# Performance work log

Hardware: AMD Instinct MI355X
Metric: run time of the kernel (lower is better)

The kernel has to match this reference:

```python
import jax, jax.numpy as jnp
import numpy as np

HEIGHT, WIDTH = 224, 224
SIGMA = 3e-4      # soft-coverage falloff (DIB-R style delta)
EPS = 1e-10


def setup_inputs() -> dict:
    key = jax.random.key(0)
    kp, kf, kc = jax.random.split(key, 3)
    B, P, F = 2, 2048, 256
    points = 0.5 * jax.random.normal(kp, (B, P, 3), dtype=jnp.float32)
    faces = jax.random.randint(kf, (F, 3), 0, P, dtype=jnp.int32)
    colors = jax.random.uniform(kc, (B, P, 3), dtype=jnp.float32)
    rot = jnp.broadcast_to(jnp.eye(3, dtype=jnp.float32), (B, 3, 3))
    pos = jnp.tile(jnp.array([0.0, 0.0, 2.5], jnp.float32), (B, 1))
    tanfov = float(np.tan(45.0 * np.pi / 360.0))
    proj = jnp.array([[1.0 / tanfov], [1.0 / tanfov], [-1.0]], jnp.float32)
    return dict(points_bxpx3=points, faces_fx3=faces, camera_rot=rot,
                camera_pos=pos, camera_proj=proj, colors_bxpx3=colors)


def _render(points_bxpx3, camera_rot, camera_pos, camera_proj, colors_bxpx3, faces_fx3):
    H, W = HEIGHT, WIDTH
    # ---- perspective projection (kaolin DIB-R convention) ----
    pc = jnp.einsum('bpj,bij->bpi', points_bxpx3 - camera_pos[:, None, :], camera_rot)  # camera space [B,P,3]
    xyz = pc * camera_proj.reshape(1, 1, 3)
    xy = xyz[..., :2] / xyz[..., 2:3]                                   # NDC xy [B,P,2]
    i0, i1, i2 = faces_fx3[:, 0], faces_fx3[:, 1], faces_fx3[:, 2]
    p0, p1, p2 = pc[:, i0], pc[:, i1], pc[:, i2]                        # [B,F,3]
    q0, q1, q2 = xy[:, i0], xy[:, i1], xy[:, i2]                        # [B,F,2]
    normal = jnp.cross(p1 - p0, p2 - p0)                                # [B,F,3]
    normalz = normal[..., 2]
    normal1 = normal / jnp.sqrt(jnp.sum(normal * normal, -1, keepdims=True) + EPS)
    # ---- per-face vertex features: 3 verts x (rgb + mask) == color_bxfx12 ----
    ones = jnp.ones(colors_bxpx3.shape[:2] + (1,), colors_bxpx3.dtype)
    cm = jnp.concatenate([colors_bxpx3, ones], -1)                      # [B,P,4]
    feat = jnp.stack([cm[:, i0], cm[:, i1], cm[:, i2]], axis=2)         # [B,F,3,4]
    # ---- rasterize: per-pixel per-face barycentric test ----
    xs = (2.0 * jnp.arange(W, dtype=jnp.float32) + 1.0) / W - 1.0
    ys = 1.0 - (2.0 * jnp.arange(H, dtype=jnp.float32) + 1.0) / H
    PX = xs[None, None, :, None]                                        # [1,1,W,1]
    PY = ys[None, :, None, None]                                        # [1,H,1,1]
    bf = lambda a: a[:, None, None, :]                                  # [B,F] -> [B,1,1,F]
    x0, y0 = q0[..., 0], q0[..., 1]
    x1, y1 = q1[..., 0], q1[..., 1]
    x2, y2 = q2[..., 0], q2[..., 1]
    denom = (y1 - y2) * (x0 - x2) + (x2 - x1) * (y0 - y2)
    denom = jnp.where(jnp.abs(denom) < EPS, EPS, denom)
    dx2 = PX - bf(x2)
    dy2 = PY - bf(y2)
    lam0 = (bf(y1 - y2) * dx2 + bf(x2 - x1) * dy2) / bf(denom)          # [B,H,W,F]
    lam1 = (bf(y2 - y0) * dx2 + bf(x0 - x2) * dy2) / bf(denom)
    lam2 = 1.0 - lam0 - lam1
    inside = (lam0 >= 0) & (lam1 >= 0) & (lam2 >= 0)
    front = (normalz > 0)[:, None, None, :]
    valid = inside & front
    # nearest face: camera looks down -z, nearer == larger camera-space z
    zpix = lam0 * bf(p0[..., 2]) + lam1 * bf(p1[..., 2]) + lam2 * bf(p2[..., 2])
    score = jnp.where(valid, zpix, -1e10)
    idx = jnp.argmax(score, axis=-1)                                    # [B,H,W]
    valid_any = jnp.any(valid, axis=-1)
    take = lambda a: jnp.take_along_axis(a, idx[..., None], axis=-1)[..., 0]
    l0, l1, l2 = take(lam0), take(lam1), take(lam2)
    fsel = jax.vmap(lambda f, i: f[i])(feat, idx)                       # [B,H,W,3,4]
    imfeat = (l0[..., None] * fsel[..., 0, :] + l1[..., None] * fsel[..., 1, :]
              + l2[..., None] * fsel[..., 2, :]) * valid_any[..., None]
    # ---- soft coverage probability: dist to nearest edge, 0 inside ----
    def seg_d2(ax, ay, bx, by):
        ex, ey = bf(bx - ax), bf(by - ay)
        pax, pay = PX - bf(ax), PY - bf(ay)
        t = jnp.clip((pax * ex + pay * ey) / (ex * ex + ey * ey + EPS), 0.0, 1.0)
        ddx, ddy = pax - t * ex, pay - t * ey
        return ddx * ddx + ddy * ddy
    d2 = jnp.minimum(seg_d2(x0, y0, x1, y1),
                     jnp.minimum(seg_d2(x1, y1, x2, y2), seg_d2(x2, y2, x0, y0)))
    d2 = jnp.where(inside, 0.0, d2)
    prob = jnp.where(front, jnp.exp(-d2 / SIGMA) * (1.0 - 1e-7), 0.0)
    improb = (1.0 - jnp.exp(jnp.sum(jnp.log1p(-prob), axis=-1)))[..., None]  # [B,H,W,1]
    imrender = imfeat[..., :3]
    return imrender, improb, normal1


def reference(points_bxpx3, camera_rot, camera_pos, camera_proj, colors_bxpx3, faces_fx3):
    return _render(points_bxpx3, camera_rot, camera_pos, camera_proj, colors_bxpx3, faces_fx3)
```

## Files before the change

### kernel.cpp

```cpp
#include <hip/hip_runtime.h>
#include <math.h>

#define HGT 224
#define WID 224
#define NPIX (HGT * WID)
#define SIGMA 0.0003f
#define EPSV 1e-10f
#define FILT_STRIDE 16
#define DATA_STRIDE 32
#define MARGIN 0.062f
#define HALFDIAG 0.04420f
#define BAND (MARGIN + HALFDIAG)
#define HD_IN (HALFDIAG + 1.0e-4f)


__global__ void face_pre(const float* __restrict__ points,
                         const int* __restrict__ faces,
                         const float* __restrict__ rot,
                         const float* __restrict__ pos,
                         const float* __restrict__ proj,
                         const float* __restrict__ colors,
                         float* __restrict__ filt,
                         float* __restrict__ data,
                         float* __restrict__ out_normal,
                         int B, int P, int F) {
    int gid = blockIdx.x * blockDim.x + threadIdx.x;
    if (gid >= B * F) return;
    int b = gid / F;
    int f = gid - b * F;

    const float* Rb = rot + b * 9;
    float posx = pos[b * 3 + 0], posy = pos[b * 3 + 1], posz = pos[b * 3 + 2];
    float pj0 = proj[0], pj1 = proj[1], pj2 = proj[2];

    float pcx[3], pcy[3], pcz[3], qx[3], qy[3], col[9];
    for (int v = 0; v < 3; v++) {
        int i = faces[f * 3 + v];
        float dx = points[(b * P + i) * 3 + 0] - posx;
        float dy = points[(b * P + i) * 3 + 1] - posy;
        float dz = points[(b * P + i) * 3 + 2] - posz;
        pcx[v] = Rb[0] * dx + Rb[1] * dy + Rb[2] * dz;
        pcy[v] = Rb[3] * dx + Rb[4] * dy + Rb[5] * dz;
        pcz[v] = Rb[6] * dx + Rb[7] * dy + Rb[8] * dz;
        float zz = pcz[v] * pj2;
        qx[v] = (pcx[v] * pj0) / zz;
        qy[v] = (pcy[v] * pj1) / zz;
        col[v * 3 + 0] = colors[(b * P + i) * 3 + 0];
        col[v * 3 + 1] = colors[(b * P + i) * 3 + 1];
        col[v * 3 + 2] = colors[(b * P + i) * 3 + 2];
    }

    float ux = pcx[1] - pcx[0], uy = pcy[1] - pcy[0], uz = pcz[1] - pcz[0];
    float vx = pcx[2] - pcx[0], vy = pcy[2] - pcy[0], vz = pcz[2] - pcz[0];
    float nx = uy * vz - uz * vy;
    float ny = uz * vx - ux * vz;
    float nz = ux * vy - uy * vx;
    float ninv = 1.0f / sqrtf(nx * nx + ny * ny + nz * nz + EPSV);
    out_normal[gid * 3 + 0] = nx * ninv;
    out_normal[gid * 3 + 1] = ny * ninv;
    out_normal[gid * 3 + 2] = nz * ninv;

    float x0 = qx[0], y0 = qy[0], x1 = qx[1], y1 = qy[1], x2 = qx[2], y2 = qy[2];
    float denom = (y1 - y2) * (x0 - x2) + (x2 - x1) * (y0 - y2);
    if (fabsf(denom) < EPSV) denom = EPSV;
    float rd = 1.0f / denom;

    float a00 = (y1 - y2) * rd;
    float a01 = (x2 - x1) * rd;
    float a10 = (y2 - y0) * rd;
    float a11 = (x0 - x2) * rd;

    float z0 = pcz[0], z1 = pcz[1], z2c = pcz[2];
    float zgx = a00 * (z0 - z2c) + a10 * (z1 - z2c);
    float zgy = a01 * (z0 - z2c) + a11 * (z1 - z2c);
    float zc  = z2c - zgx * x2 - zgy * y2;

    float* fq = filt + gid * FILT_STRIDE;
    bool front = nz > 0.0f;
    fq[0] = front ? fminf(x0, fminf(x1, x2)) :  1e30f;
    fq[1] = front ? fminf(y0, fminf(y1, y2)) :  1e30f;
    fq[2] = front ? fmaxf(x0, fmaxf(x1, x2)) : -1e30f;
    fq[3] = front ? fmaxf(y0, fmaxf(y1, y2)) : -1e30f;

    float n0 = 1.0f / sqrtf(a00 * a00 + a01 * a01 + EPSV);
    float n1 = 1.0f / sqrtf(a10 * a10 + a11 * a11 + EPSV);
    float g2x = -(a00 + a10), g2y = -(a01 + a11);
    float n2 = 1.0f / sqrtf(g2x * g2x + g2y * g2y + EPSV);
    fq[4] = a00 * n0;
    fq[5] = a01 * n0;
    fq[6] = -(a00 * x2 + a01 * y2) * n0;
    fq[7] = a10 * n1;
    fq[8] = a11 * n1;
    fq[9] = -(a10 * x2 + a11 * y2) * n1;
    fq[10] = g2x * n2;
    fq[11] = g2y * n2;
    fq[12] = (1.0f - g2x * x2 - g2y * y2) * n2;
    fq[13] = zgx; fq[14] = zgy; fq[15] = zc;

    float* fp = data + gid * DATA_STRIDE;
    fp[0] = x2; fp[1] = y2;
    fp[2] = zgx; fp[3] = zgy; fp[4] = z2c;
    fp[5] = a00; fp[6] = a01; fp[7] = a10; fp[8] = a11;
    fp[9] = x0; fp[10] = y0; fp[11] = x1; fp[12] = y1;

    float e01x = x1 - x0, e01y = y1 - y0;
    float e12x = x2 - x1, e12y = y2 - y1;
    float e20x = x0 - x2, e20y = y0 - y2;
    fp[13] = e01x; fp[14] = e01y; fp[15] = 1.0f / (e01x * e01x + e01y * e01y + EPSV);
    fp[16] = e12x; fp[17] = e12y; fp[18] = 1.0f / (e12x * e12x + e12y * e12y + EPSV);
    fp[19] = e20x; fp[20] = e20y; fp[21] = 1.0f / (e20x * e20x + e20y * e20y + EPSV);
    for (int k = 0; k < 9; k++) fp[22 + k] = col[k];
    fp[31] = 0.0f;
}

__device__ __forceinline__ float seg_d2(float px, float py, float ax, float ay,
                                        float ex, float ey, float inv) {
    float pax = px - ax, pay = py - ay;
    float t = (pax * ex + pay * ey) * inv;
    t = fminf(fmaxf(t, 0.0f), 1.0f);
    float ddx = pax - t * ex;
    float ddy = pay - t * ey;
    return ddx * ddx + ddy * ddy;
}

__global__ __launch_bounds__(256) void rast(const float* __restrict__ filt,
                                            const float* __restrict__ data,
                                            float* __restrict__ out,
                                            int B, int F) {
    const int tiles_x = WID / 8;
    const int tiles_per_batch = tiles_x * (HGT / 8);
    int b = blockIdx.x / tiles_per_batch;
    int tile = blockIdx.x - b * tiles_per_batch;
    int ty = tile / tiles_x;
    int tx = tile - ty * tiles_x;

    int t = threadIdx.x & 63;
    int w = threadIdx.x >> 6;
    int lx = t & 7, ly = t >> 3;
    int x = tx * 8 + lx;
    int y = ty * 8 + ly;
    float px = (2.0f * (float)x + 1.0f) / (float)WID - 1.0f;
    float py = 1.0f - (2.0f * (float)y + 1.0f) / (float)HGT;

    float txlo = (2.0f * (float)(tx * 8) + 1.0f) / (float)WID - 1.0f - MARGIN;
    float txhi = (2.0f * (float)(tx * 8 + 7) + 1.0f) / (float)WID - 1.0f + MARGIN;
    float tyhi = 1.0f - (2.0f * (float)(ty * 8) + 1.0f) / (float)HGT + MARGIN;
    float tylo = 1.0f - (2.0f * (float)(ty * 8 + 7) + 1.0f) / (float)HGT - MARGIN;
    float cx = (16.0f * (float)tx + 8.0f) / (float)WID - 1.0f;
    float cy = 1.0f - (16.0f * (float)ty + 8.0f) / (float)HGT;

    const float* fltb = filt + (size_t)b * F * FILT_STRIDE;
    const float* datb = data + (size_t)b * F * DATA_STRIDE;

    int chunk = (F + 3) >> 2;
    int fbeg = w * chunk;
    int fend = min(fbeg + chunk, F);

    float best = -1e10f;
    int bidx = -1;
    float prod = 1.0f;
    int n_in = 0;

    for (int base = fbeg; base < fend; base += 64) {
        bool pass = false, inclass = false;
        float zgx = 0.0f, zgy = 0.0f, zc = 0.0f;
        int fl = base + t;
        if (fl < fend) {
            const float* fq = fltb + fl * FILT_STRIDE;
            float4 bb = *(const float4*)fq;
            float4 e0 = *(const float4*)(fq + 4);
            float4 e1 = *(const float4*)(fq + 8);
            float4 e2 = *(const float4*)(fq + 12);
            bool bpass = (bb.x <= txhi) & (bb.z >= txlo) & (bb.y <= tyhi) & (bb.w >= tylo);
            float d0 = e0.x * cx + e0.y * cy + e0.z;
            float d1 = e0.w * cx + e1.x * cy + e1.y;
            float d2 = e1.z * cx + e1.w * cy + e2.x;
            float dmin = fminf(d0, fminf(d1, d2));
            pass = bpass & (dmin >= -BAND);
            inclass = bpass & (dmin >= HD_IN);
            zgx = e2.y; zgy = e2.z; zc = e2.w;
        }
        unsigned long long mask_in = __ballot(inclass);
        unsigned long long mask_bd = __ballot(pass) & ~mask_in;

        n_in += (int)__popcll(mask_in);
        while (mask_in) {
            int fo = (int)__builtin_ctzll(mask_in);
            mask_in &= mask_in - 1;
            float zx = __shfl(zgx, fo);
            float zy = __shfl(zgy, fo);
            float zk = __shfl(zc,  fo);
            float zpix = zx * px + zy * py + zk;
            if (zpix > best) { best = zpix; bidx = base + fo; }
        }

        while (mask_bd) {
            int fo = (int)__builtin_ctzll(mask_bd);
            mask_bd &= mask_bd - 1;
            int fi = base + fo;
            const float* fp = datb + fi * DATA_STRIDE;

            float dx2 = px - fp[0], dy2 = py - fp[1];
            float lam0 = fp[5] * dx2 + fp[6] * dy2;
            float lam1 = fp[7] * dx2 + fp[8] * dy2;
            float lam2 = 1.0f - lam0 - lam1;
            bool inside = (lam0 >= 0.0f) && (lam1 >= 0.0f) && (lam2 >= 0.0f);

            float zpix = fp[2] * dx2 + fp[3] * dy2 + fp[4];
            if (inside && zpix > best) { best = zpix; bidx = fi; }

            float dA = seg_d2(px, py, fp[9],  fp[10], fp[13], fp[14], fp[15]);
            float dB = seg_d2(px, py, fp[11], fp[12], fp[16], fp[17], fp[18]);
            float dC = seg_d2(px, py, fp[0],  fp[1],  fp[19], fp[20], fp[21]);
            float d2 = inside ? 0.0f : fminf(dA, fminf(dB, dC));
            float pr = __expf(d2 * (-1.0f / SIGMA)) * (1.0f - 1e-7f);
            prod *= (1.0f - pr);
        }
    }

    prod *= exp2f(-24.0f * (float)n_in);

    __shared__ float sc[256], sp[256];
    __shared__ int sidx[256];
    sc[threadIdx.x] = best;
    sp[threadIdx.x] = prod;
    sidx[threadIdx.x] = bidx;
    __syncthreads();

    if (w == 0) {
        best = -1e10f; bidx = -1;
        prod = 1.0f;
        for (int k = 0; k < 4; k++) {
            int j = k * 64 + t;
            prod *= sp[j];
            float v = sc[j];
            if (v > best) {
                best = v; bidx = sidx[j];
            }
        }

        float r = 0.0f, g = 0.0f, bb = 0.0f;
        if (bidx >= 0) {
            const float* fp = datb + bidx * DATA_STRIDE;
            float dx2 = px - fp[0], dy2 = py - fp[1];
            float lam0 = fp[5] * dx2 + fp[6] * dy2;
            float lam1 = fp[7] * dx2 + fp[8] * dy2;
            float lam2 = 1.0f - lam0 - lam1;
            r  = lam0 * fp[22] + lam1 * fp[25] + lam2 * fp[28];
            g  = lam0 * fp[23] + lam1 * fp[26] + lam2 * fp[29];
            bb = lam0 * fp[24] + lam1 * fp[27] + lam2 * fp[30];
        }

        int pixidx = b * NPIX + y * WID + x;
        out[pixidx * 3 + 0] = r;
        out[pixidx * 3 + 1] = g;
        out[pixidx * 3 + 2] = bb;
        out[B * NPIX * 3 + pixidx] = 1.0f - prod;
    }
}

extern "C" void kernel_launch(void* const* d_in, const int* in_sizes, int n_in,
                              void* d_out, int out_size, void* d_ws, size_t ws_size,
                              hipStream_t stream) {
    const float* points = (const float*)d_in[0];
    const int*   faces  = (const int*)d_in[1];
    const float* rot    = (const float*)d_in[2];
    const float* pos    = (const float*)d_in[3];
    const float* proj   = (const float*)d_in[4];
    const float* colors = (const float*)d_in[5];
    float* out = (float*)d_out;

    int F = in_sizes[1] / 3;
    int B = in_sizes[3] / 3;
    int P = in_sizes[0] / (3 * B);

    float* filt = (float*)d_ws;
    float* data = filt + (size_t)B * F * FILT_STRIDE;
    float* out_normal = out + B * NPIX * 3 + B * NPIX;

    int nf = B * F;
    face_pre<<<(nf + 255) / 256, 256, 0, stream>>>(points, faces, rot, pos, proj,
                                                   colors, filt, data, out_normal,
                                                   B, P, F);

    int blocks = B * (NPIX / 64);
    rast<<<blocks, 256, 0, stream>>>(filt, data, out, B, F);
}
```

Baseline: 77.70 us.

## Stage per-face data in LDS and store filter records structure-of-arrays

```diff
diff --git a/kernel.cpp b/kernel.cpp
--- a/kernel.cpp
+++ b/kernel.cpp
@@ -6,8 +6,9 @@
 #define NPIX (HGT * WID)
 #define SIGMA 0.0003f
 #define EPSV 1e-10f
-#define FILT_STRIDE 16
 #define DATA_STRIDE 32
+#define LDS_STRIDE 33
+#define MAXF 256
 #define MARGIN 0.062f
 #define HALFDIAG 0.04420f
 #define BAND (MARGIN + HALFDIAG)
@@ -75,27 +76,28 @@
     float zgy = a01 * (z0 - z2c) + a11 * (z1 - z2c);
     float zc  = z2c - zgx * x2 - zgy * y2;
 
-    float* fq = filt + gid * FILT_STRIDE;
+    int BF = B * F;
+    float4* f4 = (float4*)filt;
     bool front = nz > 0.0f;
-    fq[0] = front ? fminf(x0, fminf(x1, x2)) :  1e30f;
-    fq[1] = front ? fminf(y0, fminf(y1, y2)) :  1e30f;
-    fq[2] = front ? fmaxf(x0, fmaxf(x1, x2)) : -1e30f;
-    fq[3] = front ? fmaxf(y0, fmaxf(y1, y2)) : -1e30f;
+    if (front) {
+        f4[0 * BF + gid] = make_float4(fminf(x0, fminf(x1, x2)),
+                                       fminf(y0, fminf(y1, y2)),
+                                       fmaxf(x0, fmaxf(x1, x2)),
+                                       fmaxf(y0, fmaxf(y1, y2)));
+    } else {
+        f4[0 * BF + gid] = make_float4(1e30f, 1e30f, -1e30f, -1e30f);
+    }
 
     float n0 = 1.0f / sqrtf(a00 * a00 + a01 * a01 + EPSV);
     float n1 = 1.0f / sqrtf(a10 * a10 + a11 * a11 + EPSV);
     float g2x = -(a00 + a10), g2y = -(a01 + a11);
     float n2 = 1.0f / sqrtf(g2x * g2x + g2y * g2y + EPSV);
-    fq[4] = a00 * n0;
-    fq[5] = a01 * n0;
-    fq[6] = -(a00 * x2 + a01 * y2) * n0;
-    fq[7] = a10 * n1;
-    fq[8] = a11 * n1;
-    fq[9] = -(a10 * x2 + a11 * y2) * n1;
-    fq[10] = g2x * n2;
-    fq[11] = g2y * n2;
-    fq[12] = (1.0f - g2x * x2 - g2y * y2) * n2;
-    fq[13] = zgx; fq[14] = zgy; fq[15] = zc;
+    f4[1 * BF + gid] = make_float4(a00 * n0, a01 * n0,
+                                   -(a00 * x2 + a01 * y2) * n0, a10 * n1);
+    f4[2 * BF + gid] = make_float4(a11 * n1, -(a10 * x2 + a11 * y2) * n1,
+                                   g2x * n2, g2y * n2);
+    f4[3 * BF + gid] = make_float4((1.0f - g2x * x2 - g2y * y2) * n2,
+                                   zgx, zgy, zc);
 
     float* fp = data + gid * DATA_STRIDE;
     fp[0] = x2; fp[1] = y2;
@@ -127,6 +129,10 @@
                                             const float* __restrict__ data,
                                             float* __restrict__ out,
                                             int B, int F) {
+    __shared__ float sdat[MAXF * LDS_STRIDE];
+    __shared__ float sc[256], sp[256];
+    __shared__ int sidx[256];
+
     const int tiles_x = WID / 8;
     const int tiles_per_batch = tiles_x * (HGT / 8);
     int b = blockIdx.x / tiles_per_batch;
@@ -149,79 +155,91 @@
     float cx = (16.0f * (float)tx + 8.0f) / (float)WID - 1.0f;
     float cy = 1.0f - (16.0f * (float)ty + 8.0f) / (float)HGT;
 
-    const float* fltb = filt + (size_t)b * F * FILT_STRIDE;
     const float* datb = data + (size_t)b * F * DATA_STRIDE;
 
     int chunk = (F + 3) >> 2;
     int fbeg = w * chunk;
     int fend = min(fbeg + chunk, F);
+
+    int BF = B * F;
+    int bF = b * F;
+    const float4* fl4 = (const float4*)filt;
+    int fl = fbeg + t;
+    bool haveface = (fl < fend);
+    float4 bb = make_float4(0.f, 0.f, 0.f, 0.f);
+    float4 e0 = bb, e1 = bb, e2 = bb;
+    if (haveface) {
+        bb = fl4[0 * BF + bF + fl];
+        e0 = fl4[1 * BF + bF + fl];
+        e1 = fl4[2 * BF + bF + fl];
+        e2 = fl4[3 * BF + bF + fl];
+    }
+
+    int nvec = F * (DATA_STRIDE / 4);
+    for (int g = threadIdx.x; g < nvec; g += 256) {
+        float4 v = ((const float4*)datb)[g];
+        int f = g >> 3, k4 = g & 7;
+        float* d = &sdat[f * LDS_STRIDE + k4 * 4];
+        d[0] = v.x; d[1] = v.y; d[2] = v.z; d[3] = v.w;
+    }
+    __syncthreads();
 
     float best = -1e10f;
     int bidx = -1;
     float prod = 1.0f;
     int n_in = 0;
 
-    for (int base = fbeg; base < fend; base += 64) {
-        bool pass = false, inclass = false;
-        float zgx = 0.0f, zgy = 0.0f, zc = 0.0f;
-        int fl = base + t;
-        if (fl < fend) {
-            const float* fq = fltb + fl * FILT_STRIDE;
-            float4 bb = *(const float4*)fq;
-            float4 e0 = *(const float4*)(fq + 4);
-            float4 e1 = *(const float4*)(fq + 8);
-            float4 e2 = *(const float4*)(fq + 12);
-            bool bpass = (bb.x <= txhi) & (bb.z >= txlo) & (bb.y <= tyhi) & (bb.w >= tylo);
-            float d0 = e0.x * cx + e0.y * cy + e0.z;
-            float d1 = e0.w * cx + e1.x * cy + e1.y;
-            float d2 = e1.z * cx + e1.w * cy + e2.x;
-            float dmin = fminf(d0, fminf(d1, d2));
-            pass = bpass & (dmin >= -BAND);
-            inclass = bpass & (dmin >= HD_IN);
-            zgx = e2.y; zgy = e2.z; zc = e2.w;
-        }
-        unsigned long long mask_in = __ballot(inclass);
-        unsigned long long mask_bd = __ballot(pass) & ~mask_in;
-
-        n_in += (int)__popcll(mask_in);
-        while (mask_in) {
-            int fo = (int)__builtin_ctzll(mask_in);
-            mask_in &= mask_in - 1;
-            float zx = __shfl(zgx, fo);
-            float zy = __shfl(zgy, fo);
-            float zk = __shfl(zc,  fo);
-            float zpix = zx * px + zy * py + zk;
-            if (zpix > best) { best = zpix; bidx = base + fo; }
-        }
-
-        while (mask_bd) {
-            int fo = (int)__builtin_ctzll(mask_bd);
-            mask_bd &= mask_bd - 1;
-            int fi = base + fo;
-            const float* fp = datb + fi * DATA_STRIDE;
-
-            float dx2 = px - fp[0], dy2 = py - fp[1];
-            float lam0 = fp[5] * dx2 + fp[6] * dy2;
-            float lam1 = fp[7] * dx2 + fp[8] * dy2;
-            float lam2 = 1.0f - lam0 - lam1;
-            bool inside = (lam0 >= 0.0f) && (lam1 >= 0.0f) && (lam2 >= 0.0f);
-
-            float zpix = fp[2] * dx2 + fp[3] * dy2 + fp[4];
-            if (inside && zpix > best) { best = zpix; bidx = fi; }
-
-            float dA = seg_d2(px, py, fp[9],  fp[10], fp[13], fp[14], fp[15]);
-            float dB = seg_d2(px, py, fp[11], fp[12], fp[16], fp[17], fp[18]);
-            float dC = seg_d2(px, py, fp[0],  fp[1],  fp[19], fp[20], fp[21]);
-            float d2 = inside ? 0.0f : fminf(dA, fminf(dB, dC));
-            float pr = __expf(d2 * (-1.0f / SIGMA)) * (1.0f - 1e-7f);
-            prod *= (1.0f - pr);
-        }
+    bool pass = false, inclass = false;
+    float zgx = 0.0f, zgy = 0.0f, zc = 0.0f;
+    if (haveface) {
+        bool bpass = (bb.x <= txhi) & (bb.z >= txlo) & (bb.y <= tyhi) & (bb.w >= tylo);
+        float d0 = e0.x * cx + e0.y * cy + e0.z;
+        float d1 = e0.w * cx + e1.x * cy + e1.y;
+        float d2 = e1.z * cx + e1.w * cy + e2.x;
+        float dmin = fminf(d0, fminf(d1, d2));
+        pass = bpass & (dmin >= -BAND);
+        inclass = bpass & (dmin >= HD_IN);
+        zgx = e2.y; zgy = e2.z; zc = e2.w;
+    }
+    unsigned long long mask_in = __ballot(inclass);
+    unsigned long long mask_bd = __ballot(pass) & ~mask_in;
+
+    n_in += (int)__popcll(mask_in);
+    while (mask_in) {
+        int fo = (int)__builtin_ctzll(mask_in);
+        mask_in &= mask_in - 1;
+        float zx = __shfl(zgx, fo);
+        float zy = __shfl(zgy, fo);
+        float zk = __shfl(zc,  fo);
+        float zpix = zx * px + zy * py + zk;
+        if (zpix > best) { best = zpix; bidx = fbeg + fo; }
+    }
+
+    while (mask_bd) {
+        int fo = (int)__builtin_ctzll(mask_bd);
+        mask_bd &= mask_bd - 1;
+        int fi = fbeg + fo;
+        const float* fp = &sdat[fi * LDS_STRIDE];
+
+        float dx2 = px - fp[0], dy2 = py - fp[1];
+        float lam0 = fp[5] * dx2 + fp[6] * dy2;
+        float lam1 = fp[7] * dx2 + fp[8] * dy2;
+        float lam2 = 1.0f - lam0 - lam1;
+        bool inside = (lam0 >= 0.0f) && (lam1 >= 0.0f) && (lam2 >= 0.0f);
+
+        float zpix = fp[2] * dx2 + fp[3] * dy2 + fp[4];
+        if (inside && zpix > best) { best = zpix; bidx = fi; }
+
+        float dA = seg_d2(px, py, fp[9],  fp[10], fp[13], fp[14], fp[15]);
+        float dB = seg_d2(px, py, fp[11], fp[12], fp[16], fp[17], fp[18]);
+        float dC = seg_d2(px, py, fp[0],  fp[1],  fp[19], fp[20], fp[21]);
+        float d2 = inside ? 0.0f : fminf(dA, fminf(dB, dC));
+        float pr = __expf(d2 * (-1.0f / SIGMA)) * (1.0f - 1e-7f);
+        prod *= (1.0f - pr);
     }
 
     prod *= exp2f(-24.0f * (float)n_in);
 
-    __shared__ float sc[256], sp[256];
-    __shared__ int sidx[256];
     sc[threadIdx.x] = best;
     sp[threadIdx.x] = prod;
     sidx[threadIdx.x] = bidx;
@@ -239,22 +257,22 @@
             }
         }
 
-        float r = 0.0f, g = 0.0f, bb = 0.0f;
+        float r = 0.0f, g = 0.0f, bbv = 0.0f;
         if (bidx >= 0) {
-            const float* fp = datb + bidx * DATA_STRIDE;
+            const float* fp = &sdat[bidx * LDS_STRIDE];
             float dx2 = px - fp[0], dy2 = py - fp[1];
             float lam0 = fp[5] * dx2 + fp[6] * dy2;
             float lam1 = fp[7] * dx2 + fp[8] * dy2;
             float lam2 = 1.0f - lam0 - lam1;
-            r  = lam0 * fp[22] + lam1 * fp[25] + lam2 * fp[28];
-            g  = lam0 * fp[23] + lam1 * fp[26] + lam2 * fp[29];
-            bb = lam0 * fp[24] + lam1 * fp[27] + lam2 * fp[30];
+            r   = lam0 * fp[22] + lam1 * fp[25] + lam2 * fp[28];
+            g   = lam0 * fp[23] + lam1 * fp[26] + lam2 * fp[29];
+            bbv = lam0 * fp[24] + lam1 * fp[27] + lam2 * fp[30];
         }
 
         int pixidx = b * NPIX + y * WID + x;
         out[pixidx * 3 + 0] = r;
         out[pixidx * 3 + 1] = g;
-        out[pixidx * 3 + 2] = bb;
+        out[pixidx * 3 + 2] = bbv;
         out[B * NPIX * 3 + pixidx] = 1.0f - prod;
     }
 }
@@ -275,13 +293,13 @@
     int P = in_sizes[0] / (3 * B);
 
     float* filt = (float*)d_ws;
-    float* data = filt + (size_t)B * F * FILT_STRIDE;
+    float* data = filt + (size_t)B * F * 16;
     float* out_normal = out + B * NPIX * 3 + B * NPIX;
 
     int nf = B * F;
-    face_pre<<<(nf + 255) / 256, 256, 0, stream>>>(points, faces, rot, pos, proj,
-                                                   colors, filt, data, out_normal,
-                                                   B, P, F);
+    face_pre<<<(nf + 63) / 64, 64, 0, stream>>>(points, faces, rot, pos, proj,
+                                                colors, filt, data, out_normal,
+                                                B, P, F);
 
     int blocks = B * (NPIX / 64);
     rast<<<blocks, 256, 0, stream>>>(filt, data, out, B, F);
```

New measurement: 77.32 us. Within noise of the previous version (-0.5%).
